# Optimization experiments

Hardware: AMD Instinct MI355X
Metric: run time of the kernel (lower is better)

The kernel has to match this reference:

```python
import jax, jax.numpy as jnp
import numpy as np

SQRT_2_OVER_PI = 0.7978845608028654

def gelu_new(x):
    # HF 'gelu_new': 0.5*x*(1+tanh(sqrt(2/pi)*(x+0.044715*x^3)))
    return 0.5 * x * (1.0 + jnp.tanh(SQRT_2_OVER_PI * (x + 0.044715 * x * x * x)))

def phm_linear(x, phm_rule, W_left, W_right, bias, n):
    # x: [..., n*p]; phm_rule: [n, n, n]; W_left: [n, p, r]; W_right: [n, r, q]
    # H = sum_i kron(phm_rule[i], W_i), W_i = W_left[i] @ W_right[i]; y = x @ H + b
    p = x.shape[-1] // n
    W = jnp.einsum('ipk,ikq->ipq', W_left, W_right)          # [n, p, q]
    xr = x.reshape(x.shape[:-1] + (n, p))                    # [..., n, p]
    # kron(A,B)[a*p+r, c*q+s] = A[a,c]*B[r,s]
    y = jnp.einsum('...ap,iac,ipq->...cq', xr, phm_rule, W)  # [..., n, q]
    y = y.reshape(x.shape[:-1] + (n * W.shape[-1],))
    return y + bias

def setup_inputs() -> dict:
    key = jax.random.key(0)
    ks = jax.random.split(key, 7)
    B, S, D, d, n = 8, 4096, 768, 192, 4
    x = jax.random.normal(ks[0], (B, S, D), dtype=jnp.float32)
    phm_rule_d = jax.random.normal(ks[1], (n, n, n), dtype=jnp.float32) * 0.01
    W_left_d = jax.random.normal(ks[2], (n, D // n, 1), dtype=jnp.float32) * 0.05
    W_right_d = jax.random.normal(ks[3], (n, 1, d // n), dtype=jnp.float32) * 0.05
    bias_d = jnp.zeros((d,), dtype=jnp.float32)
    phm_rule_u = jax.random.normal(ks[4], (n, n, n), dtype=jnp.float32) * 0.01
    W_left_u = jax.random.normal(ks[5], (n, d // n, 1), dtype=jnp.float32) * 0.05
    W_right_u = jax.random.normal(ks[6], (n, 1, D // n), dtype=jnp.float32) * 0.05
    bias_u = jnp.zeros((D,), dtype=jnp.float32)
    return {"x": x, "phm_rule_d": phm_rule_d, "W_left_d": W_left_d, "W_right_d": W_right_d,
            "bias_d": bias_d, "phm_rule_u": phm_rule_u, "W_left_u": W_left_u,
            "W_right_u": W_right_u, "bias_u": bias_u}

def reference(x, phm_rule_d, W_left_d, W_right_d, bias_d, phm_rule_u, W_left_u, W_right_u, bias_u):
    n = phm_rule_d.shape[0]
    z = phm_linear(x, phm_rule_d, W_left_d, W_right_d, bias_d, n)
    z = gelu_new(z)
    return phm_linear(z, phm_rule_u, W_left_u, W_right_u, bias_u, n)
```

## Files before the change

kernel.cpp:

```cpp
#include <hip/hip_runtime.h>
#include <math.h>


#define SQ2PI 0.79788456080286535588f

template<int CTRL>
__device__ __forceinline__ float ror_add(float v) {
    int s = __builtin_amdgcn_update_dpp(0, __float_as_int(v), CTRL, 0xF, 0xF, true);
    return v + __int_as_float(s);
}
__device__ __forceinline__ float reduce16(float v) {
    v = ror_add<0x121>(v);
    v = ror_add<0x122>(v);
    v = ror_add<0x124>(v);
    v = ror_add<0x128>(v);
    return v;
}

__global__ __launch_bounds__(256)
void phm_fused(const float* __restrict__ x,
               const float* __restrict__ rule_d,
               const float* __restrict__ Wl_d,
               const float* __restrict__ Wr_d,
               const float* __restrict__ bias_d,
               const float* __restrict__ rule_u,
               const float* __restrict__ Wl_u,
               const float* __restrict__ Wr_u,
               const float* __restrict__ bias_u,
               float* __restrict__ out,
               int n_tokens)
{
    __shared__ __attribute__((aligned(16))) float sW[4][1536];
    __shared__ __attribute__((aligned(16))) float sLd[768];
    __shared__ __attribute__((aligned(16))) float sRu[768];
    __shared__ __attribute__((aligned(16))) float sLu[192];
    __shared__ float sRuleD[64];
    __shared__ float sRuleU[64];

    const int tid = threadIdx.x;
    for (int i = tid; i < 768; i += 256) sLd[i] = Wl_d[i];
    for (int i = tid; i < 768; i += 256) sRu[i] = Wr_u[i];
    if (tid < 192)      sLu[tid]        = Wl_u[tid];
    if (tid < 64)       sRuleD[tid]     = rule_d[tid];
    else if (tid < 128) sRuleU[tid-64]  = rule_u[tid-64];

    const int lane = tid & 63;
    const int wave = tid >> 6;
    const int a    = lane >> 4;
    const int r    = lane & 15;

    float bd[3];
    float rdw[4][3];
    float4 bu[3];
    #pragma unroll
    for (int w = 0; w < 3; ++w) bd[w] = bias_d[a*48 + 3*r + w];
    #pragma unroll
    for (int i = 0; i < 4; ++i)
        #pragma unroll
        for (int w = 0; w < 3; ++w) rdw[i][w] = Wr_d[i*48 + 3*r + w];
    #pragma unroll
    for (int u = 0; u < 3; ++u)
        bu[u] = *(const float4*)(bias_u + a*192 + 12*r + 4*u);

    __syncthreads();

    float* W = sW[wave];
    const int wid     = blockIdx.x * 4 + wave;
    const int n_waves = gridDim.x * 4;
    const int n_pairs = n_tokens >> 1;

    for (int pr = wid; pr < n_pairs; pr += n_waves) {
        const float* xp = x + (size_t)pr * 1536;

        #pragma unroll
        for (int j = 0; j < 6; ++j) {
            const float4 v = *(const float4*)(xp + (lane + 64*j) * 4);
            *(float4*)&W[(lane + 64*j) * 4] = v;
        }

        float s0[4] = {0,0,0,0}, s1[4] = {0,0,0,0};
        #pragma unroll
        for (int u = 0; u < 3; ++u) {
            const float4 xa = *(const float4*)&W[      a*192 + 12*r + 4*u];
            const float4 xb = *(const float4*)&W[768 + a*192 + 12*r + 4*u];
            #pragma unroll
            for (int i = 0; i < 4; ++i) {
                const float4 lv = *(const float4*)&sLd[i*192 + 12*r + 4*u];
                s0[i] = fmaf(xa.x, lv.x, s0[i]);  s1[i] = fmaf(xb.x, lv.x, s1[i]);
                s0[i] = fmaf(xa.y, lv.y, s0[i]);  s1[i] = fmaf(xb.y, lv.y, s1[i]);
                s0[i] = fmaf(xa.z, lv.z, s0[i]);  s1[i] = fmaf(xb.z, lv.z, s1[i]);
                s0[i] = fmaf(xa.w, lv.w, s0[i]);  s1[i] = fmaf(xb.w, lv.w, s1[i]);
            }
        }

        float tD0[4], tD1[4];
        #pragma unroll
        for (int i = 0; i < 4; ++i) {
            const float rk0 = sRuleD[i*16 + (a^0)*4 + a];
            const float rk1 = sRuleD[i*16 + (a^1)*4 + a];
            const float rk2 = sRuleD[i*16 + (a^2)*4 + a];
            const float rk3 = sRuleD[i*16 + (a^3)*4 + a];
            const float h0 = reduce16(s0[i]);
            const float h1 = reduce16(s1[i]);
            float x1 = __shfl_xor(h0, 16), x2 = __shfl_xor(h0, 32), x3 = __shfl_xor(x1, 32);
            tD0[i] = fmaf(h0, rk0, fmaf(x1, rk1, fmaf(x2, rk2, x3 * rk3)));
            x1 = __shfl_xor(h1, 16); x2 = __shfl_xor(h1, 32); x3 = __shfl_xor(x1, 32);
            tD1[i] = fmaf(h1, rk0, fmaf(x1, rk1, fmaf(x2, rk2, x3 * rk3)));
        }

        float g0[3], g1[3];
        #pragma unroll
        for (int w = 0; w < 3; ++w) {
            float z0 = bd[w], z1 = bd[w];
            #pragma unroll
            for (int i = 0; i < 4; ++i) {
                z0 = fmaf(tD0[i], rdw[i][w], z0);
                z1 = fmaf(tD1[i], rdw[i][w], z1);
            }
            const float i0 = SQ2PI * fmaf(0.044715f*z0, z0*z0, z0);
            const float i1 = SQ2PI * fmaf(0.044715f*z1, z1*z1, z1);
            const float e0 = __expf(2.0f*i0);
            const float e1 = __expf(2.0f*i1);
            g0[w] = 0.5f*z0*(1.0f + (1.0f - 2.0f/(e0 + 1.0f)));
            g1[w] = 0.5f*z1*(1.0f + (1.0f - 2.0f/(e1 + 1.0f)));
        }

        float tU0[4], tU1[4];
        #pragma unroll
        for (int i = 0; i < 4; ++i) {
            const float l0 = sLu[i*48 + 3*r + 0];
            const float l1 = sLu[i*48 + 3*r + 1];
            const float l2 = sLu[i*48 + 3*r + 2];
            const float rk0 = sRuleU[i*16 + (a^0)*4 + a];
            const float rk1 = sRuleU[i*16 + (a^1)*4 + a];
            const float rk2 = sRuleU[i*16 + (a^2)*4 + a];
            const float rk3 = sRuleU[i*16 + (a^3)*4 + a];
            float a0 = g0[0]*l0 + g0[1]*l1 + g0[2]*l2;
            float a1 = g1[0]*l0 + g1[1]*l1 + g1[2]*l2;
            const float h0 = reduce16(a0);
            const float h1 = reduce16(a1);
            float x1 = __shfl_xor(h0, 16), x2 = __shfl_xor(h0, 32), x3 = __shfl_xor(x1, 32);
            tU0[i] = fmaf(h0, rk0, fmaf(x1, rk1, fmaf(x2, rk2, x3 * rk3)));
            x1 = __shfl_xor(h1, 16); x2 = __shfl_xor(h1, 32); x3 = __shfl_xor(x1, 32);
            tU1[i] = fmaf(h1, rk0, fmaf(x1, rk1, fmaf(x2, rk2, x3 * rk3)));
        }

        #pragma unroll
        for (int u = 0; u < 3; ++u) {
            float4 ov0 = bu[u], ov1 = bu[u];
            #pragma unroll
            for (int i = 0; i < 4; ++i) {
                const float4 ru = *(const float4*)&sRu[i*192 + 12*r + 4*u];
                ov0.x = fmaf(tU0[i], ru.x, ov0.x);  ov1.x = fmaf(tU1[i], ru.x, ov1.x);
                ov0.y = fmaf(tU0[i], ru.y, ov0.y);  ov1.y = fmaf(tU1[i], ru.y, ov1.y);
                ov0.z = fmaf(tU0[i], ru.z, ov0.z);  ov1.z = fmaf(tU1[i], ru.z, ov1.z);
                ov0.w = fmaf(tU0[i], ru.w, ov0.w);  ov1.w = fmaf(tU1[i], ru.w, ov1.w);
            }
            *(float4*)&W[      a*192 + 12*r + 4*u] = ov0;
            *(float4*)&W[768 + a*192 + 12*r + 4*u] = ov1;
        }

        float* op = out + (size_t)pr * 1536;
        #pragma unroll
        for (int j = 0; j < 6; ++j) {
            const float4 v = *(const float4*)&W[(lane + 64*j) * 4];
            *(float4*)(op + (lane + 64*j) * 4) = v;
        }
    }
}

extern "C" void kernel_launch(void* const* d_in, const int* in_sizes, int n_in,
                              void* d_out, int out_size, void* d_ws, size_t ws_size,
                              hipStream_t stream) {
    const float* x      = (const float*)d_in[0];
    const float* rule_d = (const float*)d_in[1];
    const float* Wl_d   = (const float*)d_in[2];
    const float* Wr_d   = (const float*)d_in[3];
    const float* bias_d = (const float*)d_in[4];
    const float* rule_u = (const float*)d_in[5];
    const float* Wl_u   = (const float*)d_in[6];
    const float* Wr_u   = (const float*)d_in[7];
    const float* bias_u = (const float*)d_in[8];
    float* out          = (float*)d_out;

    const int n_tokens = in_sizes[0] / 768;

    phm_fused<<<dim3(1024), dim3(256), 0, stream>>>(
        x, rule_d, Wl_d, Wr_d, bias_d, rule_u, Wl_u, Wr_u, bias_u, out, n_tokens);
}
```

Before: 196.9 us.

## Load tokens directly into registers with next-pair prefetch and nontemporal stores

Drops the per-wave LDS staging buffer. Each lane now reads its 12-float slice of x straight from global memory into registers, and the loads for the next token pair are issued before computing the current one, a register double buffer. Outputs go out with nontemporal stores instead of going through LDS, bias_u moves to shared memory, and launch bounds ask for 4 blocks per CU. The per-lane 48-byte strided accesses are less coalesced than the old contiguous float4 layout, and the prefetch buffers add register pressure.

Result: slower. 347.3 us (+76.4%).

```diff
diff --git a/kernel.cpp b/kernel.cpp
--- a/kernel.cpp
+++ b/kernel.cpp
@@ -3,6 +3,8 @@
 
 
 #define SQ2PI 0.79788456080286535588f
+
+typedef float vfloat4 __attribute__((ext_vector_type(4)));
 
 template<int CTRL>
 __device__ __forceinline__ float ror_add(float v) {
@@ -17,7 +19,13 @@
     return v;
 }
 
-__global__ __launch_bounds__(256)
+__device__ __forceinline__ void nt_store4(float* p, const float4& v) {
+    vfloat4 nv;
+    nv.x = v.x; nv.y = v.y; nv.z = v.z; nv.w = v.w;
+    __builtin_nontemporal_store(nv, (vfloat4*)p);
+}
+
+__global__ __launch_bounds__(256, 4)
 void phm_fused(const float* __restrict__ x,
                const float* __restrict__ rule_d,
                const float* __restrict__ Wl_d,
@@ -30,9 +38,9 @@
                float* __restrict__ out,
                int n_tokens)
 {
-    __shared__ __attribute__((aligned(16))) float sW[4][1536];
     __shared__ __attribute__((aligned(16))) float sLd[768];
     __shared__ __attribute__((aligned(16))) float sRu[768];
+    __shared__ __attribute__((aligned(16))) float sBu[768];
     __shared__ __attribute__((aligned(16))) float sLu[192];
     __shared__ float sRuleD[64];
     __shared__ float sRuleU[64];
@@ -40,6 +48,7 @@
     const int tid = threadIdx.x;
     for (int i = tid; i < 768; i += 256) sLd[i] = Wl_d[i];
     for (int i = tid; i < 768; i += 256) sRu[i] = Wr_u[i];
+    for (int i = tid; i < 768; i += 256) sBu[i] = bias_u[i];
     if (tid < 192)      sLu[tid]        = Wl_u[tid];
     if (tid < 64)       sRuleD[tid]     = rule_d[tid];
     else if (tid < 128) sRuleU[tid-64]  = rule_u[tid-64];
@@ -48,41 +57,49 @@
     const int wave = tid >> 6;
     const int a    = lane >> 4;
     const int r    = lane & 15;
+    const int off  = 12 * lane;
 
     float bd[3];
     float rdw[4][3];
-    float4 bu[3];
     #pragma unroll
     for (int w = 0; w < 3; ++w) bd[w] = bias_d[a*48 + 3*r + w];
     #pragma unroll
     for (int i = 0; i < 4; ++i)
         #pragma unroll
         for (int w = 0; w < 3; ++w) rdw[i][w] = Wr_d[i*48 + 3*r + w];
-    #pragma unroll
-    for (int u = 0; u < 3; ++u)
-        bu[u] = *(const float4*)(bias_u + a*192 + 12*r + 4*u);
 
     __syncthreads();
 
-    float* W = sW[wave];
     const int wid     = blockIdx.x * 4 + wave;
     const int n_waves = gridDim.x * 4;
     const int n_pairs = n_tokens >> 1;
 
+    float4 A0[3], A1[3];
+    {
+        const int pr0 = (wid < n_pairs) ? wid : 0;
+        const float* xp = x + (size_t)pr0 * 1536 + off;
+        #pragma unroll
+        for (int u = 0; u < 3; ++u) {
+            A0[u] = *(const float4*)(xp + 4*u);
+            A1[u] = *(const float4*)(xp + 768 + 4*u);
+        }
+    }
+
     for (int pr = wid; pr < n_pairs; pr += n_waves) {
-        const float* xp = x + (size_t)pr * 1536;
-
-        #pragma unroll
-        for (int j = 0; j < 6; ++j) {
-            const float4 v = *(const float4*)(xp + (lane + 64*j) * 4);
-            *(float4*)&W[(lane + 64*j) * 4] = v;
+        const int nx = pr + n_waves;
+        const float* np = x + (size_t)(nx < n_pairs ? nx : pr) * 1536 + off;
+        float4 B0[3], B1[3];
+        #pragma unroll
+        for (int u = 0; u < 3; ++u) {
+            B0[u] = *(const float4*)(np + 4*u);
+            B1[u] = *(const float4*)(np + 768 + 4*u);
         }
 
         float s0[4] = {0,0,0,0}, s1[4] = {0,0,0,0};
         #pragma unroll
         for (int u = 0; u < 3; ++u) {
-            const float4 xa = *(const float4*)&W[      a*192 + 12*r + 4*u];
-            const float4 xb = *(const float4*)&W[768 + a*192 + 12*r + 4*u];
+            const float4 xa = A0[u];
+            const float4 xb = A1[u];
             #pragma unroll
             for (int i = 0; i < 4; ++i) {
                 const float4 lv = *(const float4*)&sLd[i*192 + 12*r + 4*u];
@@ -145,9 +162,11 @@
             tU1[i] = fmaf(h1, rk0, fmaf(x1, rk1, fmaf(x2, rk2, x3 * rk3)));
         }
 
-        #pragma unroll
-        for (int u = 0; u < 3; ++u) {
-            float4 ov0 = bu[u], ov1 = bu[u];
+        float* op = out + (size_t)pr * 1536 + off;
+        #pragma unroll
+        for (int u = 0; u < 3; ++u) {
+            const float4 bv = *(const float4*)&sBu[off + 4*u];
+            float4 ov0 = bv, ov1 = bv;
             #pragma unroll
             for (int i = 0; i < 4; ++i) {
                 const float4 ru = *(const float4*)&sRu[i*192 + 12*r + 4*u];
@@ -156,16 +175,12 @@
                 ov0.z = fmaf(tU0[i], ru.z, ov0.z);  ov1.z = fmaf(tU1[i], ru.z, ov1.z);
                 ov0.w = fmaf(tU0[i], ru.w, ov0.w);  ov1.w = fmaf(tU1[i], ru.w, ov1.w);
             }
-            *(float4*)&W[      a*192 + 12*r + 4*u] = ov0;
-            *(float4*)&W[768 + a*192 + 12*r + 4*u] = ov1;
-        }
-
-        float* op = out + (size_t)pr * 1536;
-        #pragma unroll
-        for (int j = 0; j < 6; ++j) {
-            const float4 v = *(const float4*)&W[(lane + 64*j) * 4];
-            *(float4*)(op + (lane + 64*j) * 4) = v;
-        }
+            nt_store4(op + 4*u,       ov0);
+            nt_store4(op + 768 + 4*u, ov1);
+        }
+
+        #pragma unroll
+        for (int u = 0; u < 3; ++u) { A0[u] = B0[u]; A1[u] = B1[u]; }
     }
 }
 
```
